# Performance work log

Measured on AMD Instinct MI355X. Metric: run time of the kernel, lower is better.

The kernel has to match this reference:

```python
import jax, jax.numpy as jnp
import numpy as np

N_NODES = 50000
N_EDGES = 100000
NODE_DIM = 6
EDGE_DIM = 4
H = 64        # hidden_dim
HEADS = 4
T = 3         # n_iterations
RED = 16      # CBAM reduction ratio
Z_VALUES = np.array([7.98, 22.98, 38.98, 53.98, 89.98, 180.48], np.float32)


def _ln(x, g, b, eps=1e-5):
    mu = jnp.mean(x, -1, keepdims=True)
    v = jnp.mean((x - mu) ** 2, -1, keepdims=True)
    return (x - mu) * jax.lax.rsqrt(v + eps) * g + b


def _conv1d(x, w, b, pad):
    y = jax.lax.conv_general_dilated(x, w, (1,), [(pad, pad)],
                                     dimension_numbers=('NCH', 'OIH', 'NCH'))
    return y + b[None, :, None]


def _cbam(x, w1, b1, w2, b2, cw1, cb1, cw2, cb2):
    # channel attention: pool over node dim -> [1, 2H] -> MLP -> sigmoid
    cat = jnp.concatenate([x.max(0, keepdims=True), x.mean(0, keepdims=True)], 1)
    cw = jax.nn.sigmoid(jnp.maximum(cat @ w1 + b1, 0.0) @ w2 + b2)  # [1, H]
    x = x * cw
    # spatial attention: pool over feature dim -> conv1d stack over node axis
    sp = jnp.stack([x.max(-1), x.mean(-1)], 0)[None]                # [1, 2, N]
    s = jnp.maximum(_conv1d(sp, cw1, cb1, 2), 0.0)
    s = jax.nn.sigmoid(_conv1d(s, cw2, cb2, 1))                     # [1, 1, N]
    return x * s[0, 0][:, None]


def _forward(x, edge_attr, z_table, W_node, b_node, W_edge, b_edge,
             cn_w1, cn_b1, cn_w2, cn_b2, cn_cw1, cn_cb1, cn_cw2, cn_cb2,
             ce_w1, ce_b1, ce_w2, ce_b2, ce_cw1, ce_cb1, ce_cw2, ce_cb2,
             ln_comb_g, ln_comb_b, Wq, bq, Wk, bk, Wv, bv, Wskip, bskip,
             ln_tc_g, ln_tc_b, Wpn, bpn, Wpe, bpe, Wg, bg,
             Wc1, bc1, Wc2, bc2, edge_index, z_keys):
    n = x.shape[0]
    # bidirectional edges
    src = jnp.concatenate([edge_index[0], edge_index[1]])
    dst = jnp.concatenate([edge_index[1], edge_index[0]])
    eab = jnp.concatenate([edge_attr, edge_attr], 0)
    rel = x[src, :3] - x[dst, :3]

    # z embedding lookup (non-matching z -> index 0, matching torch default)
    zint = jnp.round(x[:, 2]).astype(jnp.int32)
    zidx = jnp.argmax(zint[:, None] == z_keys[None, :], 1)

    nf = jnp.maximum(x @ W_node + b_node, 0.0) + z_table[zidx]
    nf = _cbam(nf, cn_w1, cn_b1, cn_w2, cn_b2, cn_cw1, cn_cb1, cn_cw2, cn_cb2)
    ef = jnp.maximum(jnp.concatenate([eab, rel], 1) @ W_edge + b_edge, 0.0)
    ef = _cbam(ef, ce_w1, ce_b1, ce_w2, ce_b2, ce_cw1, ce_cb1, ce_cw2, ce_cb2)

    scale = float(1.0 / np.sqrt(H))
    for i in range(T):
        x0, e0 = nf, ef
        agg = jax.ops.segment_sum(ef, dst, num_segments=n)
        comb = _ln(jnp.concatenate([nf, agg - nf], 1), ln_comb_g[i], ln_comb_b[i])
        # TransformerConv (PyG): q at dst, k/v at src, segment softmax over dst
        q = (comb @ Wq[i] + bq[i]).reshape(n, HEADS, H)
        k = (comb @ Wk[i] + bk[i]).reshape(n, HEADS, H)
        v = (comb @ Wv[i] + bv[i]).reshape(n, HEADS, H)
        logits = jnp.sum(q[dst] * k[src], -1) * scale           # [2E, HEADS]
        m = jax.ops.segment_max(logits, dst, num_segments=n)
        p = jnp.exp(logits - m[dst])
        denom = jax.ops.segment_sum(p, dst, num_segments=n)
        alpha = p / denom[dst]
        out = jax.ops.segment_sum(alpha[..., None] * v[src], dst, num_segments=n)
        out = out.reshape(n, HEADS * H) + comb @ Wskip[i] + bskip[i]
        out = _ln(out, ln_tc_g[i], ln_tc_b[i])
        npj = out @ Wpn[i] + bpn[i]
        epj = out[src] @ Wpe[i] + bpe[i]
        g = jax.nn.sigmoid(jnp.concatenate([x0, npj], 1) @ Wg[i] + bg[i])
        nf = x0 * g + npj * (1.0 - g)
        g2 = jax.nn.sigmoid(jnp.concatenate([e0, epj], 1) @ Wg[i] + bg[i])
        ef = e0 * g2 + epj * (1.0 - g2)

    s_idx, e_idx = edge_index[0], edge_index[1]
    clf = jnp.concatenate([nf[s_idx], nf[e_idx]], 1)
    return (jnp.maximum(clf @ Wc1 + bc1, 0.0) @ Wc2 + bc2)[:, 0]


def setup_inputs() -> dict:
    key = jax.random.key(0)
    ks = iter(jax.random.split(key, 80))
    def nrm(shape, s=0.05):
        return jax.random.normal(next(ks), shape, jnp.float32) * s
    x = jax.random.normal(next(ks), (N_NODES, NODE_DIM), jnp.float32)
    zch = jax.random.randint(next(ks), (N_NODES,), 0, len(Z_VALUES))
    x = x.at[:, 2].set(jnp.asarray(Z_VALUES)[zch])
    edge_index = jax.random.randint(next(ks), (2, N_EDGES), 0, N_NODES)
    edge_attr = jax.random.normal(next(ks), (N_EDGES, EDGE_DIM), jnp.float32)
    z_keys = jnp.asarray(np.round(Z_VALUES).astype(np.int32))
    HH, r = HEADS * H, H // RED
    def zeros(*s):
        return jnp.zeros(s, jnp.float32)
    inp = dict(
        x=x, edge_attr=edge_attr, edge_index=edge_index, z_keys=z_keys,
        z_table=nrm((len(Z_VALUES), H)),
        W_node=nrm((NODE_DIM, H)), b_node=zeros(H),
        W_edge=nrm((EDGE_DIM + 3, H)), b_edge=zeros(H),
        cn_w1=nrm((2 * H, r)), cn_b1=zeros(r), cn_w2=nrm((r, H)), cn_b2=zeros(H),
        cn_cw1=nrm((1, 2, 5)), cn_cb1=zeros(1), cn_cw2=nrm((1, 1, 3)), cn_cb2=zeros(1),
        ce_w1=nrm((2 * H, r)), ce_b1=zeros(r), ce_w2=nrm((r, H)), ce_b2=zeros(H),
        ce_cw1=nrm((1, 2, 5)), ce_cb1=zeros(1), ce_cw2=nrm((1, 1, 3)), ce_cb2=zeros(1),
        ln_comb_g=jnp.ones((T, 2 * H), jnp.float32), ln_comb_b=zeros(T, 2 * H),
        Wq=nrm((T, 2 * H, HH)), bq=zeros(T, HH),
        Wk=nrm((T, 2 * H, HH)), bk=zeros(T, HH),
        Wv=nrm((T, 2 * H, HH)), bv=zeros(T, HH),
        Wskip=nrm((T, 2 * H, HH)), bskip=zeros(T, HH),
        ln_tc_g=jnp.ones((T, HH), jnp.float32), ln_tc_b=zeros(T, HH),
        Wpn=nrm((T, HH, H)), bpn=zeros(T, H),
        Wpe=nrm((T, HH, H)), bpe=zeros(T, H),
        Wg=nrm((T, 2 * H, H)), bg=zeros(T, H),
        Wc1=nrm((2 * H, H)), bc1=zeros(H), Wc2=nrm((H, 1)), bc2=zeros(1),
    )
    return inp


def reference(x, edge_attr, edge_index, z_keys, z_table, W_node, b_node, W_edge, b_edge,
              cn_w1, cn_b1, cn_w2, cn_b2, cn_cw1, cn_cb1, cn_cw2, cn_cb2,
              ce_w1, ce_b1, ce_w2, ce_b2, ce_cw1, ce_cb1, ce_cw2, ce_cb2,
              ln_comb_g, ln_comb_b, Wq, bq, Wk, bk, Wv, bv, Wskip, bskip,
              ln_tc_g, ln_tc_b, Wpn, bpn, Wpe, bpe, Wg, bg, Wc1, bc1, Wc2, bc2):
    return _forward(x, edge_attr, z_table, W_node, b_node, W_edge, b_edge,
                    cn_w1, cn_b1, cn_w2, cn_b2, cn_cw1, cn_cb1, cn_cw2, cn_cb2,
                    ce_w1, ce_b1, ce_w2, ce_b2, ce_cw1, ce_cb1, ce_cw2, ce_cb2,
                    ln_comb_g, ln_comb_b, Wq, bq, Wk, bk, Wv, bv, Wskip, bskip,
                    ln_tc_g, ln_tc_b, Wpn, bpn, Wpe, bpe, Wg, bg,
                    Wc1, bc1, Wc2, bc2, edge_index, z_keys)
```

## Files before the change

kernel.cpp:

```cpp
#include <hip/hip_runtime.h>


#define LN_EPS 1e-5f
#define PBLK 512

typedef __attribute__((ext_vector_type(8))) short bf16x8;
typedef __attribute__((ext_vector_type(4))) float f32x4;

static __device__ __forceinline__ float wsum(float v) {
#pragma unroll
  for (int d = 32; d > 0; d >>= 1) v += __shfl_xor(v, d);
  return v;
}
static __device__ __forceinline__ float sigm(float x) { return 1.0f / (1.0f + __expf(-x)); }
static __device__ __forceinline__ unsigned short f2bf(float f) {
  unsigned int u = __float_as_uint(f);
  u += 0x7FFFu + ((u >> 16) & 1u);
  return (unsigned short)(u >> 16);
}
static __device__ __forceinline__ float bf2f(unsigned short b) {
  return __uint_as_float(((unsigned int)b) << 16);
}
static __device__ __forceinline__ float4 ld4v(const float* p) { return *(const float4*)p; }
static __device__ __forceinline__ float4 ld4v(const unsigned short* p) {
// ... 71 lines not shown
    }
    if (i < nblk) boff[i] = carry + sc - v;
    carry += __shfl(sc, 63);
  }
  if (lane == 0) off[n] = carry;
}

__global__ __launch_bounds__(256) void k_scan3(int* __restrict__ off, const int* __restrict__ boff, int n) {
  int i = blockIdx.x * 256 + threadIdx.x;
  if (i < n) off[i] += boff[i >> 10];
}

__global__ __launch_bounds__(256) void k_scatter(const int* __restrict__ ei, const int* __restrict__ off,
                                                 int* __restrict__ cur, int* __restrict__ pinv,
                                                 int* __restrict__ slist, int E) {
  int e = blockIdx.x * 256 + threadIdx.x;
  if (e >= 2 * E) return;
  int d = (e < E) ? ei[E + e] : ei[e - E];
  int pos = atomicAdd(&cur[d], 1);
  int base = off[d] + pos;
  pinv[e] = base;
  slist[base] = ei[e];
}

__global__ __launch_bounds__(256) void k_packW(
    const float* __restrict__ Wq, const float* __restrict__ Wk, const float* __restrict__ Wv,
    const float* __restrict__ Ws, const float* __restrict__ bq, const float* __restrict__ bk,
    const float* __restrict__ bv, const float* __restrict__ bs,
    const float* __restrict__ Wpn, const float* __restrict__ Wpe,
    const float* __restrict__ bpn, const float* __restrict__ bpe,
    const float* __restrict__ Wg, const float* __restrict__ Wc1,
    unsigned short* __restrict__ W1t, float* __restrict__ bias1,
    unsigned short* __restrict__ B2t, float* __restrict__ bias2,
    unsigned short* __restrict__ Wg1t, unsigned short* __restrict__ Wc1t) {
  const int S1 = 3 * 1024 * 128, S2 = 3 * 1024, S3 = 3 * 256 * 256, S4 = 3 * 256;
  const int S5 = 3 * 64 * 64, S6 = 2 * 64 * 64;
  int idx = blockIdx.x * 256 + threadIdx.x;
  if (idx < S1) {
    int i = idx / 131072, r = idx % 131072;
    int col = r >> 7, k = r & 127;
    int m = col >> 8, cc = col & 255;
    const float* W = (m == 0) ? Wq : (m == 1) ? Wk : (m == 2) ? Wv : Ws;
    W1t[idx] = f2bf(W[i * 32768 + k * 256 + cc]);
  } else if (idx < S1 + S2) {
    int j = idx - S1;
    int i = j >> 10, col = j & 1023;
    int m = col >> 8, cc = col & 255;
    const float* bsrc = (m == 0) ? bq : (m == 1) ? bk : (m == 2) ? bv : bs;
    bias1[j] = bsrc[i * 256 + cc];
  } else if (idx < S1 + S2 + S3) {
    int j = idx - S1 - S2;
    int i = j / 65536, r = j % 65536;
    int col = r >> 8, k = r & 255;
    float v;
    if (col < 64) v = Wpn[i * 16384 + k * 64 + col];
    else if (col < 128) v = Wpe[i * 16384 + k * 64 + (col - 64)];
    else {
      const float* Wsrc = (col < 192) ? Wpn : Wpe;
      int cc = col & 63;
      float acc = 0.f;
      for (int jj = 0; jj < 64; ++jj)
        acc = fmaf(Wsrc[i * 16384 + k * 64 + jj], Wg[i * 8192 + (64 + jj) * 64 + cc], acc);
      v = acc;
    }
    B2t[j] = f2bf(v);
  } else if (idx < S1 + S2 + S3 + S4) {
    int j = idx - S1 - S2 - S3;
    int i = j >> 8, col = j & 255;
    float v;
    if (col < 64) v = bpn[i * 64 + col];
    else if (col < 128) v = bpe[i * 64 + col - 64];
    else {
      const float* bsrc = (col < 192) ? bpn : bpe;
      int cc = col & 63;
      float acc = 0.f;
      for (int jj = 0; jj < 64; ++jj)
        acc = fmaf(bsrc[i * 64 + jj], Wg[i * 8192 + (64 + jj) * 64 + cc], acc);
      v = acc;
    }
    bias2[j] = v;
  } else if (idx < S1 + S2 + S3 + S4 + S5) {
    int j = idx - S1 - S2 - S3 - S4;
    int i = j / 4096, r = j % 4096;
    int col = r >> 6, k = r & 63;
    Wg1t[j] = f2bf(Wg[i * 8192 + k * 64 + col]);
  } else if (idx < S1 + S2 + S3 + S4 + S5 + S6) {
    int j = idx - S1 - S2 - S3 - S4 - S5;
    int h = j / 4096, r = j % 4096;
    int col = r >> 6, k = r & 63;
    Wc1t[j] = f2bf(Wc1[(h * 64 + k) * 64 + col]);
  }
}

__global__ __launch_bounds__(256) void k_node_embed(
    const float* __restrict__ x, const int* __restrict__ zk, const float* __restrict__ zt,
    const float* __restrict__ Wn, const float* __restrict__ bn, float* __restrict__ nf, int N) {
  int n = blockIdx.x * 4 + (threadIdx.x >> 6);
  int lane = threadIdx.x & 63;
  if (n >= N) return;
  const float* xr = x + (size_t)n * 6;
  float acc = bn[lane];
#pragma unroll
  for (int d = 0; d < 6; ++d) acc = fmaf(xr[d], Wn[d * 64 + lane], acc);
  int zi = __float2int_rn(xr[2]);
  int idx = 0;
#pragma unroll
  for (int t = 5; t >= 0; --t)
    if (zi == zk[t]) idx = t;
  nf[(size_t)n * 64 + lane] = fmaxf(acc, 0.0f) + zt[idx * 64 + lane];
}

__global__ __launch_bounds__(256) void k_edge_embed(
    const float* __restrict__ x, const float* __restrict__ ea, const int* __restrict__ ei,
    const float* __restrict__ We, const float* __restrict__ be,
    unsigned short* __restrict__ ef, int E) {
  int e = blockIdx.x * 4 + (threadIdx.x >> 6);
  int lane = threadIdx.x & 63;
  if (e >= 2 * E) return;
  int e0 = (e < E) ? e : e - E;
  int s = ei[e];
  int d = (e < E) ? ei[E + e] : ei[e - E];
  const float* ar = ea + (size_t)e0 * 4;
  const float* xs = x + (size_t)s * 6;
  const float* xd = x + (size_t)d * 6;
  float in[7];
  in[0] = ar[0]; in[1] = ar[1]; in[2] = ar[2]; in[3] = ar[3];
  in[4] = xs[0] - xd[0]; in[5] = xs[1] - xd[1]; in[6] = xs[2] - xd[2];
// ... 124 lines not shown
  __syncthreads();
  int o = base + threadIdx.x;
  if (o < n) {
    float a = b2[0] + tl[threadIdx.x] * w2[0] + tl[threadIdx.x + 1] * w2[1] + tl[threadIdx.x + 2] * w2[2];
    s[o] = sigm(a);
  }
}

__global__ __launch_bounds__(256) void k_row_scale(float* __restrict__ buf, int n, const float* __restrict__ s) {
  int i4 = blockIdx.x * 256 + threadIdx.x;
  if (i4 >= n * 16) return;
  int r = i4 >> 4;
  float sc = s[r];
  float4 v = ld4v(buf + (size_t)i4 * 4);
  v.x *= sc; v.y *= sc; v.z *= sc; v.w *= sc;
  st4v(buf + (size_t)i4 * 4, v);
}

__global__ __launch_bounds__(256) void k_row_scale_perm(const unsigned short* __restrict__ src, int n,
                                                        const float* __restrict__ s,
                                                        const int* __restrict__ pinv,
                                                        unsigned short* __restrict__ dst) {
  int i4 = blockIdx.x * 256 + threadIdx.x;
  if (i4 >= n * 16) return;
  int r = i4 >> 4, c4 = (i4 & 15) * 4;
  float sc = s[r];
  float4 v = ld4v(src + (size_t)r * 64 + c4);
  v.x *= sc; v.y *= sc; v.z *= sc; v.w *= sc;
  st4v(dst + (size_t)pinv[r] * 64 + c4, v);
}

__global__ __launch_bounds__(256) void k_aggcomb(const unsigned short* __restrict__ efc,
                                                 const float* __restrict__ nf,
                                                 const int* __restrict__ off,
                                                 unsigned short* __restrict__ comb, const float* __restrict__ g,
                                                 const float* __restrict__ b, int N) {
  int n = blockIdx.x * 4 + (threadIdx.x >> 6);
  int lane = threadIdx.x & 63;
  if (n >= N) return;
  float agg = 0.0f;
  int i0 = off[n], i1 = off[n + 1];
  for (int idx = i0; idx < i1; ++idx) agg += bf2f(efc[(size_t)idx * 64 + lane]);
  float y0 = nf[(size_t)n * 64 + lane];
  float y1 = agg - y0;
  float s1 = wsum(y0 + y1);
  float s2 = wsum(y0 * y0 + y1 * y1);
  float mu = s1 * (1.0f / 128.0f);
  float var = s2 * (1.0f / 128.0f) - mu * mu;
  float rs = rsqrtf(fmaxf(var, 0.0f) + LN_EPS);
  comb[(size_t)n * 128 + lane] = f2bf((y0 - mu) * rs * g[lane] + b[lane]);
  comb[(size_t)n * 128 + 64 + lane] = f2bf((y1 - mu) * rs * g[64 + lane] + b[64 + lane]);
}

template <int MODE>
__global__ __launch_bounds__(256) void gemm_mfma(
    const unsigned short* __restrict__ A, int M, int K,
    const unsigned short* __restrict__ Bt, const float* __restrict__ bias,
    unsigned short* __restrict__ outQ, unsigned short* __restrict__ outK,
    unsigned short* __restrict__ outS) {
  __shared__ unsigned short shmem[128 * 136];
  unsigned short* As = shmem;
  unsigned short* Bs = shmem + 128 * 64;
  const int tid = threadIdx.x;
  int bm, bn;
  if (MODE == 0) {
    int cpx = gridDim.x >> 3;
    int wgid = (blockIdx.x & 7) * cpx + (blockIdx.x >> 3);
    bm = (wgid >> 3) * 128;
    bn = (wgid & 7) * 128;
  } else {
    bm = blockIdx.x * 128;
    bn = blockIdx.y * 128;
  }
  const int wid = tid >> 6, lane = tid & 63;
  const int wr = (wid >> 1) * 64, wc = (wid & 1) * 64;
  const int lrow = lane & 15, lkb = (lane >> 4) * 8;
  f32x4 acc[4][4];
#pragma unroll
  for (int m = 0; m < 4; ++m)
#pragma unroll
    for (int n = 0; n < 4; ++n) acc[m][n] = (f32x4){0.f, 0.f, 0.f, 0.f};

  for (int k0 = 0; k0 < K; k0 += 64) {
#pragma unroll
    for (int l = 0; l < 4; ++l) {
      int c = tid + l * 256;
      int row = c >> 3, kc = (c & 7) * 8;
      int sw = row * 64 + (kc ^ ((row & 7) << 3));
      int grow = bm + row;
      bf16x8 v = {0, 0, 0, 0, 0, 0, 0, 0};
      if (grow < M) v = *(const bf16x8*)(A + (size_t)grow * K + k0 + kc);
      *(bf16x8*)&As[sw] = v;
      int gcol = bn + row;
      *(bf16x8*)&Bs[sw] = *(const bf16x8*)(Bt + (size_t)gcol * K + k0 + kc);
    }
    __syncthreads();
#pragma unroll
    for (int ks = 0; ks < 2; ++ks) {
      const int ke = ks * 32 + lkb;
      bf16x8 af[4], bfr[4];
#pragma unroll
      for (int m = 0; m < 4; ++m) {
        int row = wr + m * 16 + lrow;
        af[m] = *(const bf16x8*)&As[row * 64 + (ke ^ ((row & 7) << 3))];
      }
#pragma unroll
      for (int n = 0; n < 4; ++n) {
        int col = wc + n * 16 + lrow;
        bfr[n] = *(const bf16x8*)&Bs[col * 64 + (ke ^ ((col & 7) << 3))];
      }
#pragma unroll
      for (int m = 0; m < 4; ++m)
#pragma unroll
        for (int n = 0; n < 4; ++n)
          acc[m][n] = __builtin_amdgcn_mfma_f32_16x16x32_bf16(af[m], bfr[n], acc[m][n], 0, 0, 0);
    }
    __syncthreads();
  }

  const int colw = lane & 15, rq = (lane >> 4) * 4;
  unsigned short* Cs = shmem;
#pragma unroll
  for (int m = 0; m < 4; ++m) {
#pragma unroll
    for (int n = 0; n < 4; ++n) {
      int col = wc + n * 16 + colw;
      float bv = bias[bn + col];
#pragma unroll
      for (int r = 0; r < 4; ++r) {
        int row = wr + m * 16 + rq + r;
        Cs[row * 136 + col] = f2bf(acc[m][n][r] + bv);
      }
    }
  }
  __syncthreads();
  const int rsub = tid >> 4, c8 = (tid & 15) * 8;
#pragma unroll
  for (int i = 0; i < 8; ++i) {
    int row = i * 16 + rsub;
    int grow = bm + row;
    if (grow >= M) continue;
    uint4 v = *(const uint4*)&Cs[row * 136 + c8];
    if (MODE == 1) {
      *(uint4*)(outQ + (size_t)grow * 256 + bn + c8) = v;
    } else {
      const int proj = bn >> 8;
      int cc = (bn & 255) + c8;
      if (proj == 0) *(uint4*)(outQ + (size_t)grow * 256 + cc) = v;
      else if (proj == 1) *(uint4*)(outK + (size_t)grow * 512 + cc) = v;
      else if (proj == 2) *(uint4*)(outK + (size_t)grow * 512 + 256 + cc) = v;
      else *(uint4*)(outS + (size_t)grow * 256 + cc) = v;
    }
  }
}

template <int UPD>
__global__ __launch_bounds__(256) void gemm_gate(
    const void* __restrict__ Av, int M, const unsigned short* __restrict__ Wt,
    const unsigned short* __restrict__ P, const float* __restrict__ bgv,
    const int* __restrict__ srcl, void* __restrict__ updv) {
  __shared__ unsigned short As[128 * 64];
  __shared__ unsigned short Ws[64 * 64];
  const int tid = threadIdx.x;
  const int bm = blockIdx.x * 128;
  if (UPD == 2) {
    const unsigned short* Ab = (const unsigned short*)Av;
#pragma unroll
    for (int l = 0; l < 4; ++l) {
      int u = tid + l * 256;
      int row = u >> 3, kc = (u & 7) * 8;
      int grow = bm + row;
      bf16x8 v = {0, 0, 0, 0, 0, 0, 0, 0};
      if (grow < M) v = *(const bf16x8*)(Ab + (size_t)grow * 64 + kc);
      *(bf16x8*)&As[row * 64 + (kc ^ ((row & 7) << 3))] = v;
    }
  } else {
    const float* Af = (const float*)Av;
#pragma unroll
    for (int l = 0; l < 8; ++l) {
      int u = tid + l * 256;
      int row = u >> 4, k4 = (u & 15) << 2;
      int grow = bm + row;
      float4 v = make_float4(0.f, 0.f, 0.f, 0.f);
      if (grow < M) v = *(const float4*)(Af + (size_t)grow * 64 + k4);
      union { unsigned short h[4]; uint2 q; } pk;
      pk.h[0] = f2bf(v.x); pk.h[1] = f2bf(v.y); pk.h[2] = f2bf(v.z); pk.h[3] = f2bf(v.w);
      *(uint2*)&As[row * 64 + (k4 ^ ((row & 7) << 3))] = pk.q;
    }
  }
#pragma unroll
  for (int l = 0; l < 2; ++l) {
    int u = tid + l * 256;
    int row = u >> 3, kc = (u & 7) * 8;
    *(bf16x8*)&Ws[row * 64 + (kc ^ ((row & 7) << 3))] = *(const bf16x8*)(Wt + row * 64 + kc);
  }
  __syncthreads();
  const int wid = tid >> 6, lane = tid & 63;
  const int wr = wid * 32;
  const int lrow = lane & 15, lkb = (lane >> 4) * 8;
  f32x4 acc[2][4];
#pragma unroll
  for (int m = 0; m < 2; ++m)
#pragma unroll
    for (int n = 0; n < 4; ++n) acc[m][n] = (f32x4){0.f, 0.f, 0.f, 0.f};
#pragma unroll
  for (int ks = 0; ks < 2; ++ks) {
    const int ke = ks * 32 + lkb;
    bf16x8 af[2], wf[4];
#pragma unroll
    for (int m = 0; m < 2; ++m) {
      int row = wr + m * 16 + lrow;
      af[m] = *(const bf16x8*)&As[row * 64 + (ke ^ ((row & 7) << 3))];
    }
#pragma unroll
    for (int n = 0; n < 4; ++n) {
      int col = n * 16 + lrow;
      wf[n] = *(const bf16x8*)&Ws[col * 64 + (ke ^ ((col & 7) << 3))];
    }
#pragma unroll
    for (int m = 0; m < 2; ++m)
#pragma unroll
      for (int n = 0; n < 4; ++n)
        acc[m][n] = __builtin_amdgcn_mfma_f32_16x16x32_bf16(af[m], wf[n], acc[m][n], 0, 0, 0);
  }
  const int colw = lane & 15, rq = (lane >> 4) * 4;
#pragma unroll
  for (int m = 0; m < 2; ++m) {
#pragma unroll
    for (int r = 0; r < 4; ++r) {
      int e = bm + wr + m * 16 + rq + r;
      if (e >= M) continue;
      if (UPD == 0) {
        float* upd = (float*)updv;
#pragma unroll
        for (int n = 0; n < 4; ++n) upd[(size_t)e * 64 + n * 16 + colw] = acc[m][n][r];
      } else if (UPD == 1) {
        float* upd = (float*)updv;
        const unsigned short* Pr = P + (size_t)e * 256;
#pragma unroll
        for (int n = 0; n < 4; ++n) {
          int c = n * 16 + colw;
          float g = sigm(acc[m][n][r] + bf2f(Pr[128 + c]) + bgv[c]);
          size_t oi = (size_t)e * 64 + c;
          upd[oi] = upd[oi] * g + bf2f(Pr[c]) * (1.0f - g);
        }
      } else {
        unsigned short* upd = (unsigned short*)updv;
        int s = srcl[e];
        const unsigned short* Pr = P + (size_t)s * 256;
#pragma unroll
        for (int n = 0; n < 4; ++n) {
          int c = n * 16 + colw;
          float g = sigm(acc[m][n][r] + bf2f(Pr[192 + c]) + bgv[c]);
          size_t oi = (size_t)e * 64 + c;
          float vA = bf2f(upd[oi]);
          upd[oi] = f2bf(vA * g + bf2f(Pr[64 + c]) * (1.0f - g));
        }
      }
    }
  }
}

__global__ __launch_bounds__(256) void k_attn(const unsigned short* __restrict__ qo,
                                              const unsigned short* __restrict__ kv,
                                              const unsigned short* __restrict__ skipb, const int* __restrict__ off,
                                              const int* __restrict__ slist,
                                              unsigned short* __restrict__ aob,
                                              const float* __restrict__ g, const float* __restrict__ b, int N) {
  int n = blockIdx.x * 4 + (threadIdx.x >> 6);
  int lane = threadIdx.x & 63;
  if (n >= N) return;
  union { uint2 u; unsigned short h[4]; } qq;
  qq.u = *(const uint2*)(qo + (size_t)n * 256 + 4 * lane);
  float q0 = bf2f(qq.h[0]), q1 = bf2f(qq.h[1]), q2 = bf2f(qq.h[2]), q3 = bf2f(qq.h[3]);
  float m = -INFINITY, lsum = 0.f;
  float a0 = 0.f, a1 = 0.f, a2 = 0.f, a3 = 0.f;
  int i0 = off[n], i1 = off[n + 1];
  int idx = i0;
  for (; idx + 4 <= i1; idx += 4) {
    int s0 = slist[idx], s1 = slist[idx + 1], s2 = slist[idx + 2], s3 = slist[idx + 3];
    const unsigned short* kb0 = kv + (size_t)s0 * 512;
    const unsigned short* kb1 = kv + (size_t)s1 * 512;
    const unsigned short* kb2 = kv + (size_t)s2 * 512;
    const unsigned short* kb3 = kv + (size_t)s3 * 512;
    union { uint2 u; unsigned short h[4]; } kk0, vv0, kk1, vv1, kk2, vv2, kk3, vv3;
    kk0.u = *(const uint2*)(kb0 + 4 * lane); vv0.u = *(const uint2*)(kb0 + 256 + 4 * lane);
    kk1.u = *(const uint2*)(kb1 + 4 * lane); vv1.u = *(const uint2*)(kb1 + 256 + 4 * lane);
    kk2.u = *(const uint2*)(kb2 + 4 * lane); vv2.u = *(const uint2*)(kb2 + 256 + 4 * lane);
    kk3.u = *(const uint2*)(kb3 + 4 * lane); vv3.u = *(const uint2*)(kb3 + 256 + 4 * lane);
    float d0 = q0 * bf2f(kk0.h[0]) + q1 * bf2f(kk0.h[1]) + q2 * bf2f(kk0.h[2]) + q3 * bf2f(kk0.h[3]);
    float d1 = q0 * bf2f(kk1.h[0]) + q1 * bf2f(kk1.h[1]) + q2 * bf2f(kk1.h[2]) + q3 * bf2f(kk1.h[3]);
    float d2 = q0 * bf2f(kk2.h[0]) + q1 * bf2f(kk2.h[1]) + q2 * bf2f(kk2.h[2]) + q3 * bf2f(kk2.h[3]);
    float d3 = q0 * bf2f(kk3.h[0]) + q1 * bf2f(kk3.h[1]) + q2 * bf2f(kk3.h[2]) + q3 * bf2f(kk3.h[3]);
#pragma unroll
    for (int dd = 1; dd < 16; dd <<= 1) {
      d0 += __shfl_xor(d0, dd);
      d1 += __shfl_xor(d1, dd);
      d2 += __shfl_xor(d2, dd);
      d3 += __shfl_xor(d3, dd);
    }
    d0 *= 0.125f; d1 *= 0.125f; d2 *= 0.125f; d3 *= 0.125f;
    float nm, sc, p;
    nm = fmaxf(m, d0); sc = __expf(m - nm); p = __expf(d0 - nm);
    lsum = lsum * sc + p;
    a0 = fmaf(p, bf2f(vv0.h[0]), a0 * sc); a1 = fmaf(p, bf2f(vv0.h[1]), a1 * sc);
    a2 = fmaf(p, bf2f(vv0.h[2]), a2 * sc); a3 = fmaf(p, bf2f(vv0.h[3]), a3 * sc);
    m = nm;
    nm = fmaxf(m, d1); sc = __expf(m - nm); p = __expf(d1 - nm);
    lsum = lsum * sc + p;
    a0 = fmaf(p, bf2f(vv1.h[0]), a0 * sc); a1 = fmaf(p, bf2f(vv1.h[1]), a1 * sc);
    a2 = fmaf(p, bf2f(vv1.h[2]), a2 * sc); a3 = fmaf(p, bf2f(vv1.h[3]), a3 * sc);
    m = nm;
    nm = fmaxf(m, d2); sc = __expf(m - nm); p = __expf(d2 - nm);
    lsum = lsum * sc + p;
    a0 = fmaf(p, bf2f(vv2.h[0]), a0 * sc); a1 = fmaf(p, bf2f(vv2.h[1]), a1 * sc);
    a2 = fmaf(p, bf2f(vv2.h[2]), a2 * sc); a3 = fmaf(p, bf2f(vv2.h[3]), a3 * sc);
    m = nm;
    nm = fmaxf(m, d3); sc = __expf(m - nm); p = __expf(d3 - nm);
    lsum = lsum * sc + p;
    a0 = fmaf(p, bf2f(vv3.h[0]), a0 * sc); a1 = fmaf(p, bf2f(vv3.h[1]), a1 * sc);
    a2 = fmaf(p, bf2f(vv3.h[2]), a2 * sc); a3 = fmaf(p, bf2f(vv3.h[3]), a3 * sc);
    m = nm;
  }
  for (; idx + 2 <= i1; idx += 2) {
    int sA = slist[idx], sB = slist[idx + 1];
    const unsigned short* kbA = kv + (size_t)sA * 512;
    const unsigned short* kbB = kv + (size_t)sB * 512;
    union { uint2 u; unsigned short h[4]; } kkA, vvA, kkB, vvB;
    kkA.u = *(const uint2*)(kbA + 4 * lane); vvA.u = *(const uint2*)(kbA + 256 + 4 * lane);
    kkB.u = *(const uint2*)(kbB + 4 * lane); vvB.u = *(const uint2*)(kbB + 256 + 4 * lane);
    float dA = q0 * bf2f(kkA.h[0]) + q1 * bf2f(kkA.h[1]) + q2 * bf2f(kkA.h[2]) + q3 * bf2f(kkA.h[3]);
    float dB = q0 * bf2f(kkB.h[0]) + q1 * bf2f(kkB.h[1]) + q2 * bf2f(kkB.h[2]) + q3 * bf2f(kkB.h[3]);
#pragma unroll
    for (int dd = 1; dd < 16; dd <<= 1) {
      dA += __shfl_xor(dA, dd);
      dB += __shfl_xor(dB, dd);
    }
    dA *= 0.125f; dB *= 0.125f;
    float nm, sc, p;
    nm = fmaxf(m, dA); sc = __expf(m - nm); p = __expf(dA - nm);
    lsum = lsum * sc + p;
    a0 = fmaf(p, bf2f(vvA.h[0]), a0 * sc); a1 = fmaf(p, bf2f(vvA.h[1]), a1 * sc);
    a2 = fmaf(p, bf2f(vvA.h[2]), a2 * sc); a3 = fmaf(p, bf2f(vvA.h[3]), a3 * sc);
    m = nm;
    nm = fmaxf(m, dB); sc = __expf(m - nm); p = __expf(dB - nm);
    lsum = lsum * sc + p;
    a0 = fmaf(p, bf2f(vvB.h[0]), a0 * sc); a1 = fmaf(p, bf2f(vvB.h[1]), a1 * sc);
    a2 = fmaf(p, bf2f(vvB.h[2]), a2 * sc); a3 = fmaf(p, bf2f(vvB.h[3]), a3 * sc);
    m = nm;
  }
  if (idx < i1) {
    int s = slist[idx];
    const unsigned short* kb = kv + (size_t)s * 512;
    union { uint2 u; unsigned short h[4]; } kk, vv;
    kk.u = *(const uint2*)(kb + 4 * lane);
    vv.u = *(const uint2*)(kb + 256 + 4 * lane);
    float d = q0 * bf2f(kk.h[0]) + q1 * bf2f(kk.h[1]) + q2 * bf2f(kk.h[2]) + q3 * bf2f(kk.h[3]);
#pragma unroll
    for (int dd = 1; dd < 16; dd <<= 1) d += __shfl_xor(d, dd);
    d *= 0.125f;
    float nm = fmaxf(m, d);
    float sc = __expf(m - nm);
    float p = __expf(d - nm);
    lsum = lsum * sc + p;
    a0 = fmaf(p, bf2f(vv.h[0]), a0 * sc);
    a1 = fmaf(p, bf2f(vv.h[1]), a1 * sc);
    a2 = fmaf(p, bf2f(vv.h[2]), a2 * sc);
    a3 = fmaf(p, bf2f(vv.h[3]), a3 * sc);
    m = nm;
  }
  union { uint2 u; unsigned short h[4]; } sb;
  sb.u = *(const uint2*)(skipb + (size_t)n * 256 + 4 * lane);
  float inv = (lsum > 0.f) ? 1.0f / lsum : 0.f;
  float v0 = bf2f(sb.h[0]) + a0 * inv;
  float v1 = bf2f(sb.h[1]) + a1 * inv;
  float v2 = bf2f(sb.h[2]) + a2 * inv;
  float v3 = bf2f(sb.h[3]) + a3 * inv;
  float s1 = wsum(v0 + v1 + v2 + v3);
  float s2 = wsum(v0 * v0 + v1 * v1 + v2 * v2 + v3 * v3);
  float mu = s1 * (1.0f / 256.0f);
  float var = s2 * (1.0f / 256.0f) - mu * mu;
  float rs = rsqrtf(fmaxf(var, 0.0f) + LN_EPS);
  float4 g4 = *(const float4*)(g + 4 * lane);
  float4 b4 = *(const float4*)(b + 4 * lane);
  union { uint2 u; unsigned short h[4]; } ob;
  ob.h[0] = f2bf((v0 - mu) * rs * g4.x + b4.x);
  ob.h[1] = f2bf((v1 - mu) * rs * g4.y + b4.y);
  ob.h[2] = f2bf((v2 - mu) * rs * g4.z + b4.z);
  ob.h[3] = f2bf((v3 - mu) * rs * g4.w + b4.w);
  *(uint2*)(aob + (size_t)n * 256 + 4 * lane) = ob.u;
}

__global__ __launch_bounds__(256) void k_clf_pair(const float* __restrict__ ABt, const float* __restrict__ ABb,
                                                  const int* __restrict__ ei, const float* __restrict__ bc1,
                                                  const float* __restrict__ Wc2, const float* __restrict__ bc2,
                                                  float* __restrict__ out, int E) {
  int e = blockIdx.x * 4 + (threadIdx.x >> 6);
  int lane = threadIdx.x & 63;
  if (e >= E) return;
  int s = ei[e], t = ei[E + e];
  float h = fmaxf(ABt[(size_t)s * 64 + lane] + ABb[(size_t)t * 64 + lane] + bc1[lane], 0.0f);
  float r = wsum(h * Wc2[lane]);
  if (lane == 0) out[e] = r + bc2[0];
}

extern "C" void kernel_launch(void* const* d_in, const int* in_sizes, int n_in,
                              void* d_out, int out_size, void* d_ws, size_t ws_size,
                              hipStream_t stream) {
  const float* x = (const float*)d_in[0];
  const float* edge_attr = (const float*)d_in[1];
  const int* ei = (const int*)d_in[2];
  const int* zk = (const int*)d_in[3];
  const float* z_table = (const float*)d_in[4];
  const float* W_node = (const float*)d_in[5];
  const float* b_node = (const float*)d_in[6];
  const float* W_edge = (const float*)d_in[7];
  const float* b_edge = (const float*)d_in[8];
  const float* cn_w1 = (const float*)d_in[9];
  const float* cn_b1 = (const float*)d_in[10];
  const float* cn_w2 = (const float*)d_in[11];
  const float* cn_b2 = (const float*)d_in[12];
  const float* cn_cw1 = (const float*)d_in[13];
// ... 21 lines not shown
  const float* ln_tc_g = (const float*)d_in[35];
  const float* ln_tc_b = (const float*)d_in[36];
  const float* Wpn = (const float*)d_in[37];
  const float* bpn = (const float*)d_in[38];
  const float* Wpe = (const float*)d_in[39];
  const float* bpe = (const float*)d_in[40];
  const float* Wg = (const float*)d_in[41];
  const float* bg = (const float*)d_in[42];
  const float* Wc1 = (const float*)d_in[43];
  const float* bc1 = (const float*)d_in[44];
  const float* Wc2 = (const float*)d_in[45];
  const float* bc2 = (const float*)d_in[46];
  float* out = (float*)d_out;

  const int N = in_sizes[0] / 6;
  const int E = in_sizes[2] / 2;
  const int E2 = 2 * E;

  char* p = (char*)d_ws;
  auto carve = [&](size_t bytes) -> void* {
    void* r = (void*)p;
    p += (bytes + 255) & ~(size_t)255;
    return r;
  };
  unsigned short* qo = (unsigned short*)carve((size_t)N * 256 * 2);
  unsigned short* skipb = (unsigned short*)carve((size_t)N * 256 * 2);
  unsigned short* kvb = (unsigned short*)carve((size_t)N * 512 * 2);
  unsigned short* aob = (unsigned short*)carve((size_t)N * 256 * 2);
  unsigned short* efb = (unsigned short*)carve((size_t)E2 * 64 * 2);
  unsigned short* efc = (unsigned short*)carve((size_t)E2 * 64 * 2);
  float* nf = (float*)carve((size_t)N * 64 * 4);
  unsigned short* comb = (unsigned short*)carve((size_t)N * 128 * 2);
  unsigned short* W1t = (unsigned short*)carve((size_t)3 * 1024 * 128 * 2);
  float* bias1 = (float*)carve((size_t)3 * 1024 * 4);
  unsigned short* B2t = (unsigned short*)carve((size_t)3 * 256 * 256 * 2);
  float* bias2 = (float*)carve((size_t)3 * 256 * 4);
  unsigned short* Wg1t = (unsigned short*)carve((size_t)3 * 64 * 64 * 2);
  unsigned short* Wc1t = (unsigned short*)carve((size_t)2 * 64 * 64 * 2);
  int* cnt = (int*)carve((size_t)N * 4);
  int* cur = (int*)carve((size_t)N * 4);
  int* off = (int*)carve((size_t)(N + 1) * 4);
  int* pinv = (int*)carve((size_t)E2 * 4);
  int* slist = (int*)carve((size_t)E2 * 4);
  int* bsum = (int*)carve((size_t)256 * 4);
  int* boff = (int*)carve((size_t)256 * 4);
  float* pm = (float*)carve((size_t)PBLK * 64 * 4);
  float* ps = (float*)carve((size_t)PBLK * 64 * 4);
  float* cwv = (float*)carve(64 * 4);
  float* spmax = (float*)carve((size_t)E2 * 4);
  float* spmean = (float*)carve((size_t)E2 * 4);
  float* sconv = (float*)carve((size_t)E2 * 4);
  size_t need = (size_t)(p - (char*)d_ws);

  unsigned short* Pb = skipb;
  float* ABt = (float*)aob;
  float* ABb = (float*)aob + (size_t)N * 64;

  auto cdiv = [](int a, int b) { return (a + b - 1) / b; };

  if (ws_size < need) {
    k_sentinel<<<cdiv(E, 256), 256, 0, stream>>>(out, E);
    return;
  }

  k_zero2<<<cdiv(N, 256), 256, 0, stream>>>(cnt, cur, N);
  k_hist<<<cdiv(E2, 256), 256, 0, stream>>>(ei, cnt, E);
  const int nblk = cdiv(N, 1024);
  k_scan1<<<nblk, 256, 0, stream>>>(cnt, off, bsum, N);
  k_scan2<<<1, 64, 0, stream>>>(bsum, boff, off, N, nblk);
  k_scan3<<<cdiv(N, 256), 256, 0, stream>>>(off, boff, N);
  k_scatter<<<cdiv(E2, 256), 256, 0, stream>>>(ei, off, cur, pinv, slist, E);

  const int PACK = 3 * 1024 * 128 + 3 * 1024 + 3 * 256 * 256 + 3 * 256 + 3 * 64 * 64 + 2 * 64 * 64;
  k_packW<<<cdiv(PACK, 256), 256, 0, stream>>>(Wq, Wk, Wv, Wskip, bq, bk, bv, bskip,
                                               Wpn, Wpe, bpn, bpe, Wg, Wc1,
                                               W1t, bias1, B2t, bias2, Wg1t, Wc1t);

  k_node_embed<<<cdiv(N, 4), 256, 0, stream>>>(x, zk, z_table, W_node, b_node, nf, N);
  k_edge_embed<<<cdiv(E2, 4), 256, 0, stream>>>(x, edge_attr, ei, W_edge, b_edge, efb, E);

  k_pool_partial<float><<<PBLK, 256, 0, stream>>>(nf, N, pm, ps);
  k_pool_final<<<1, 256, 0, stream>>>(pm, ps, N, PBLK, cn_w1, cn_b1, cn_w2, cn_b2, cwv);
  k_chan_sp<float><<<cdiv(N, 16), 256, 0, stream>>>(nf, N, cwv, spmax, spmean);
  k_conv<<<cdiv(N, 256), 256, 0, stream>>>(spmax, spmean, N, cn_cw1, cn_cb1, cn_cw2, cn_cb2, sconv);
  k_row_scale<<<cdiv(N * 16, 256), 256, 0, stream>>>(nf, N, sconv);

  k_pool_partial<unsigned short><<<PBLK, 256, 0, stream>>>(efb, E2, pm, ps);
  k_pool_final<<<1, 256, 0, stream>>>(pm, ps, E2, PBLK, ce_w1, ce_b1, ce_w2, ce_b2, cwv);
  k_chan_sp<unsigned short><<<cdiv(E2, 16), 256, 0, stream>>>(efb, E2, cwv, spmax, spmean);
  k_conv<<<cdiv(E2, 256), 256, 0, stream>>>(spmax, spmean, E2, ce_cw1, ce_cb1, ce_cw2, ce_cb2, sconv);
  k_row_scale_perm<<<cdiv(E2 * 16, 256), 256, 0, stream>>>(efb, E2, sconv, pinv, efc);

  const int gqkvs = cdiv(N, 128) * 8;
  dim3 gp(cdiv(N, 128), 2);
  for (int i = 0; i < 3; ++i) {
    k_aggcomb<<<cdiv(N, 4), 256, 0, stream>>>(efc, nf, off, comb,
                                              ln_comb_g + (size_t)i * 128, ln_comb_b + (size_t)i * 128, N);
    gemm_mfma<0><<<gqkvs, 256, 0, stream>>>(comb, N, 128, W1t + (size_t)i * 131072,
                                            bias1 + (size_t)i * 1024, qo, kvb, skipb);
    k_attn<<<cdiv(N, 4), 256, 0, stream>>>(qo, kvb, skipb, off, slist, aob,
                                           ln_tc_g + (size_t)i * 256, ln_tc_b + (size_t)i * 256, N);
    gemm_mfma<1><<<gp, 256, 0, stream>>>(aob, N, 256, B2t + (size_t)i * 65536,
                                         bias2 + (size_t)i * 256, Pb, nullptr, nullptr);
    gemm_gate<1><<<cdiv(N, 128), 256, 0, stream>>>(nf, N, Wg1t + (size_t)i * 4096, Pb,
                                                   bg + (size_t)i * 64, nullptr, nf);
    gemm_gate<2><<<cdiv(E2, 128), 256, 0, stream>>>(efc, E2, Wg1t + (size_t)i * 4096, Pb,
                                                    bg + (size_t)i * 64, slist, efc);
  }

  gemm_gate<0><<<cdiv(N, 128), 256, 0, stream>>>(nf, N, Wc1t, nullptr, nullptr, nullptr, ABt);
  gemm_gate<0><<<cdiv(N, 128), 256, 0, stream>>>(nf, N, Wc1t + 4096, nullptr, nullptr, nullptr, ABb);
  k_clf_pair<<<cdiv(E, 4), 256, 0, stream>>>(ABt, ABb, ei, bc1, Wc2, bc2, out, E);
  (void)out_size;
  (void)n_in;
}
```

Baseline: 714.7 us.

## Fuse node gate update into projection GEMM and drop online-softmax max tracking

The P projection GEMM and the node gate update become one kernel, gemm_p. Blocks with y=0 compute the node gate GEMM and apply the gated update to nf directly, and blocks with y=1 write only the edge-side projections into a compact 128-wide buffer. This removes one kernel launch per iteration and halves the P buffer traffic. The attention kernel also drops the running-max rescaling of online softmax and exponentiates the scaled scores directly, which risks overflow if scores get large.

After: 697.9 us. 1.02x faster.

```diff
diff --git a/kernel.cpp b/kernel.cpp
--- a/kernel.cpp
+++ b/kernel.cpp
@@ -147,12 +147,12 @@
     int j = idx - S1 - S2;
     int i = j / 65536, r = j % 65536;
     int col = r >> 8, k = r & 255;
+    int half = col >> 6, cc = col & 63;
     float v;
-    if (col < 64) v = Wpn[i * 16384 + k * 64 + col];
-    else if (col < 128) v = Wpe[i * 16384 + k * 64 + (col - 64)];
+    if (half == 0) v = Wpn[i * 16384 + k * 64 + cc];
+    else if (half == 2) v = Wpe[i * 16384 + k * 64 + cc];
     else {
-      const float* Wsrc = (col < 192) ? Wpn : Wpe;
-      int cc = col & 63;
+      const float* Wsrc = (half == 1) ? Wpn : Wpe;
       float acc = 0.f;
       for (int jj = 0; jj < 64; ++jj)
         acc = fmaf(Wsrc[i * 16384 + k * 64 + jj], Wg[i * 8192 + (64 + jj) * 64 + cc], acc);
@@ -162,12 +162,12 @@
   } else if (idx < S1 + S2 + S3 + S4) {
     int j = idx - S1 - S2 - S3;
     int i = j >> 8, col = j & 255;
+    int half = col >> 6, cc = col & 63;
     float v;
-    if (col < 64) v = bpn[i * 64 + col];
-    else if (col < 128) v = bpe[i * 64 + col - 64];
+    if (half == 0) v = bpn[i * 64 + cc];
+    else if (half == 2) v = bpe[i * 64 + cc];
     else {
-      const float* bsrc = (col < 192) ? bpn : bpe;
-      int cc = col & 63;
+      const float* bsrc = (half == 1) ? bpn : bpe;
       float acc = 0.f;
       for (int jj = 0; jj < 64; ++jj)
         acc = fmaf(bsrc[i * 64 + jj], Wg[i * 8192 + (64 + jj) * 64 + cc], acc);
@@ -398,7 +398,6 @@
   comb[(size_t)n * 128 + 64 + lane] = f2bf((y1 - mu) * rs * g[64 + lane] + b[64 + lane]);
 }
 
-template <int MODE>
 __global__ __launch_bounds__(256) void gemm_mfma(
     const unsigned short* __restrict__ A, int M, int K,
     const unsigned short* __restrict__ Bt, const float* __restrict__ bias,
@@ -408,16 +407,10 @@
   unsigned short* As = shmem;
   unsigned short* Bs = shmem + 128 * 64;
   const int tid = threadIdx.x;
-  int bm, bn;
-  if (MODE == 0) {
-    int cpx = gridDim.x >> 3;
-    int wgid = (blockIdx.x & 7) * cpx + (blockIdx.x >> 3);
-    bm = (wgid >> 3) * 128;
-    bn = (wgid & 7) * 128;
-  } else {
-    bm = blockIdx.x * 128;
-    bn = blockIdx.y * 128;
-  }
+  int cpx = gridDim.x >> 3;
+  int wgid = (blockIdx.x & 7) * cpx + (blockIdx.x >> 3);
+  int bm = (wgid >> 3) * 128;
+  int bn = (wgid & 7) * 128;
   const int wid = tid >> 6, lane = tid & 63;
   const int wr = (wid >> 1) * 64, wc = (wid & 1) * 64;
   const int lrow = lane & 15, lkb = (lane >> 4) * 8;
@@ -487,15 +480,164 @@
     int grow = bm + row;
     if (grow >= M) continue;
     uint4 v = *(const uint4*)&Cs[row * 136 + c8];
-    if (MODE == 1) {
-      *(uint4*)(outQ + (size_t)grow * 256 + bn + c8) = v;
-    } else {
-      const int proj = bn >> 8;
-      int cc = (bn & 255) + c8;
-      if (proj == 0) *(uint4*)(outQ + (size_t)grow * 256 + cc) = v;
-      else if (proj == 1) *(uint4*)(outK + (size_t)grow * 512 + cc) = v;
-      else if (proj == 2) *(uint4*)(outK + (size_t)grow * 512 + 256 + cc) = v;
-      else *(uint4*)(outS + (size_t)grow * 256 + cc) = v;
+    const int proj = bn >> 8;
+    int cc = (bn & 255) + c8;
+    if (proj == 0) *(uint4*)(outQ + (size_t)grow * 256 + cc) = v;
+    else if (proj == 1) *(uint4*)(outK + (size_t)grow * 512 + cc) = v;
+    else if (proj == 2) *(uint4*)(outK + (size_t)grow * 512 + 256 + cc) = v;
+    else *(uint4*)(outS + (size_t)grow * 256 + cc) = v;
+  }
+}
+
+__global__ __launch_bounds__(256) void gemm_p(
+    const unsigned short* __restrict__ aob, float* __restrict__ nf, int N,
+    const unsigned short* __restrict__ B2t, const float* __restrict__ bias2,
+    const unsigned short* __restrict__ Wg1t, const float* __restrict__ bgv,
+    unsigned short* __restrict__ Pe) {
+  __shared__ unsigned short shmem[128 * 136];
+  unsigned short* As = shmem;
+  unsigned short* Bs = shmem + 128 * 64;
+  const int tid = threadIdx.x;
+  const int bm = blockIdx.x * 128;
+  const bool nodeblk = (blockIdx.y == 0);
+  const int wid = tid >> 6, lane = tid & 63;
+  const int lrow = lane & 15, lkb = (lane >> 4) * 8;
+
+  f32x4 accS[2][4];
+  if (nodeblk) {
+#pragma unroll
+    for (int l = 0; l < 8; ++l) {
+      int u = tid + l * 256;
+      int row = u >> 4, k4 = (u & 15) << 2;
+      int grow = bm + row;
+      float4 v = make_float4(0.f, 0.f, 0.f, 0.f);
+      if (grow < N) v = *(const float4*)(nf + (size_t)grow * 64 + k4);
+      union { unsigned short h[4]; uint2 q; } pk;
+      pk.h[0] = f2bf(v.x); pk.h[1] = f2bf(v.y); pk.h[2] = f2bf(v.z); pk.h[3] = f2bf(v.w);
+      *(uint2*)&As[row * 64 + (k4 ^ ((row & 7) << 3))] = pk.q;
+    }
+#pragma unroll
+    for (int l = 0; l < 2; ++l) {
+      int u = tid + l * 256;
+      int row = u >> 3, kc = (u & 7) * 8;
+      *(bf16x8*)&Bs[row * 64 + (kc ^ ((row & 7) << 3))] = *(const bf16x8*)(Wg1t + row * 64 + kc);
+    }
+    __syncthreads();
+    const int wrS = wid * 32;
+#pragma unroll
+    for (int m = 0; m < 2; ++m)
+#pragma unroll
+      for (int n = 0; n < 4; ++n) accS[m][n] = (f32x4){0.f, 0.f, 0.f, 0.f};
+#pragma unroll
+    for (int ks = 0; ks < 2; ++ks) {
+      const int ke = ks * 32 + lkb;
+      bf16x8 af[2], wf[4];
+#pragma unroll
+      for (int m = 0; m < 2; ++m) {
+        int row = wrS + m * 16 + lrow;
+        af[m] = *(const bf16x8*)&As[row * 64 + (ke ^ ((row & 7) << 3))];
+      }
+#pragma unroll
+      for (int n = 0; n < 4; ++n) {
+        int col = n * 16 + lrow;
+        wf[n] = *(const bf16x8*)&Bs[col * 64 + (ke ^ ((col & 7) << 3))];
+      }
+#pragma unroll
+      for (int m = 0; m < 2; ++m)
+#pragma unroll
+        for (int n = 0; n < 4; ++n)
+          accS[m][n] = __builtin_amdgcn_mfma_f32_16x16x32_bf16(af[m], wf[n], accS[m][n], 0, 0, 0);
+    }
+    __syncthreads();
+  }
+
+  const int cbase = nodeblk ? 0 : 128;
+  const int wr = (wid >> 1) * 64, wc = (wid & 1) * 64;
+  f32x4 acc[4][4];
+#pragma unroll
+  for (int m = 0; m < 4; ++m)
+#pragma unroll
+    for (int n = 0; n < 4; ++n) acc[m][n] = (f32x4){0.f, 0.f, 0.f, 0.f};
+  for (int k0 = 0; k0 < 256; k0 += 64) {
+#pragma unroll
+    for (int l = 0; l < 4; ++l) {
+      int c = tid + l * 256;
+      int row = c >> 3, kc = (c & 7) * 8;
+      int sw = row * 64 + (kc ^ ((row & 7) << 3));
+      int grow = bm + row;
+      bf16x8 v = {0, 0, 0, 0, 0, 0, 0, 0};
+      if (grow < N) v = *(const bf16x8*)(aob + (size_t)grow * 256 + k0 + kc);
+      *(bf16x8*)&As[sw] = v;
+      *(bf16x8*)&Bs[sw] = *(const bf16x8*)(B2t + (size_t)(cbase + row) * 256 + k0 + kc);
+    }
+    __syncthreads();
+#pragma unroll
+    for (int ks = 0; ks < 2; ++ks) {
+      const int ke = ks * 32 + lkb;
+      bf16x8 af[4], bfr[4];
+#pragma unroll
+      for (int m = 0; m < 4; ++m) {
+        int row = wr + m * 16 + lrow;
+        af[m] = *(const bf16x8*)&As[row * 64 + (ke ^ ((row & 7) << 3))];
+      }
+#pragma unroll
+      for (int n = 0; n < 4; ++n) {
+        int col = wc + n * 16 + lrow;
+        bfr[n] = *(const bf16x8*)&Bs[col * 64 + (ke ^ ((col & 7) << 3))];
+      }
+#pragma unroll
+      for (int m = 0; m < 4; ++m)
+#pragma unroll
+        for (int n = 0; n < 4; ++n)
+          acc[m][n] = __builtin_amdgcn_mfma_f32_16x16x32_bf16(af[m], bfr[n], acc[m][n], 0, 0, 0);
+    }
+    __syncthreads();
+  }
+
+  const int colw = lane & 15, rq = (lane >> 4) * 4;
+  unsigned short* Cs = shmem;
+#pragma unroll
+  for (int m = 0; m < 4; ++m) {
+#pragma unroll
+    for (int n = 0; n < 4; ++n) {
+      int col = wc + n * 16 + colw;
+      float bv = bias2[cbase + col];
+#pragma unroll
+      for (int r = 0; r < 4; ++r) {
+        int row = wr + m * 16 + rq + r;
+        Cs[row * 136 + col] = f2bf(acc[m][n][r] + bv);
+      }
+    }
+  }
+  __syncthreads();
+
+  if (nodeblk) {
+    const int wrS = wid * 32;
+#pragma unroll
+    for (int m = 0; m < 2; ++m) {
+#pragma unroll
+      for (int r = 0; r < 4; ++r) {
+        int row = wrS + m * 16 + rq + r;
+        int grow = bm + row;
+        if (grow >= N) continue;
+#pragma unroll
+        for (int n = 0; n < 4; ++n) {
+          int c = n * 16 + colw;
+          float g = sigm(accS[m][n][r] + bf2f(Cs[row * 136 + 64 + c]) + bgv[c]);
+          size_t oi = (size_t)grow * 64 + c;
+          float old = nf[oi];
+          nf[oi] = old * g + bf2f(Cs[row * 136 + c]) * (1.0f - g);
+        }
+      }
+    }
+  } else {
+    const int rsub = tid >> 4, c8 = (tid & 15) * 8;
+#pragma unroll
+    for (int i = 0; i < 8; ++i) {
+      int row = i * 16 + rsub;
+      int grow = bm + row;
+      if (grow >= N) continue;
+      *(uint4*)(Pe + (size_t)grow * 128 + c8) = *(const uint4*)&Cs[row * 136 + c8];
     }
   }
 }
@@ -580,27 +722,17 @@
         float* upd = (float*)updv;
 #pragma unroll
         for (int n = 0; n < 4; ++n) upd[(size_t)e * 64 + n * 16 + colw] = acc[m][n][r];
-      } else if (UPD == 1) {
-        float* upd = (float*)updv;
-        const unsigned short* Pr = P + (size_t)e * 256;
-#pragma unroll
-        for (int n = 0; n < 4; ++n) {
-          int c = n * 16 + colw;
-          float g = sigm(acc[m][n][r] + bf2f(Pr[128 + c]) + bgv[c]);
-          size_t oi = (size_t)e * 64 + c;
-          upd[oi] = upd[oi] * g + bf2f(Pr[c]) * (1.0f - g);
-        }
       } else {
         unsigned short* upd = (unsigned short*)updv;
         int s = srcl[e];
-        const unsigned short* Pr = P + (size_t)s * 256;
+        const unsigned short* Pr = P + (size_t)s * 128;
 #pragma unroll
         for (int n = 0; n < 4; ++n) {
           int c = n * 16 + colw;
-          float g = sigm(acc[m][n][r] + bf2f(Pr[192 + c]) + bgv[c]);
+          float g = sigm(acc[m][n][r] + bf2f(Pr[64 + c]) + bgv[c]);
           size_t oi = (size_t)e * 64 + c;
           float vA = bf2f(upd[oi]);
-          upd[oi] = f2bf(vA * g + bf2f(Pr[64 + c]) * (1.0f - g));
+          upd[oi] = f2bf(vA * g + bf2f(Pr[c]) * (1.0f - g));
         }
       }
     }
@@ -619,7 +751,7 @@
   union { uint2 u; unsigned short h[4]; } qq;
   qq.u = *(const uint2*)(qo + (size_t)n * 256 + 4 * lane);
   float q0 = bf2f(qq.h[0]), q1 = bf2f(qq.h[1]), q2 = bf2f(qq.h[2]), q3 = bf2f(qq.h[3]);
-  float m = -INFINITY, lsum = 0.f;
+  float lsum = 0.f;
   float a0 = 0.f, a1 = 0.f, a2 = 0.f, a3 = 0.f;
   int i0 = off[n], i1 = off[n + 1];
   int idx = i0;
@@ -645,57 +777,21 @@
       d2 += __shfl_xor(d2, dd);
       d3 += __shfl_xor(d3, dd);
     }
-    d0 *= 0.125f; d1 *= 0.125f; d2 *= 0.125f; d3 *= 0.125f;
-    float nm, sc, p;
-    nm = fmaxf(m, d0); sc = __expf(m - nm); p = __expf(d0 - nm);
-    lsum = lsum * sc + p;
-    a0 = fmaf(p, bf2f(vv0.h[0]), a0 * sc); a1 = fmaf(p, bf2f(vv0.h[1]), a1 * sc);
-    a2 = fmaf(p, bf2f(vv0.h[2]), a2 * sc); a3 = fmaf(p, bf2f(vv0.h[3]), a3 * sc);
-    m = nm;
-    nm = fmaxf(m, d1); sc = __expf(m - nm); p = __expf(d1 - nm);
-    lsum = lsum * sc + p;
-    a0 = fmaf(p, bf2f(vv1.h[0]), a0 * sc); a1 = fmaf(p, bf2f(vv1.h[1]), a1 * sc);
-    a2 = fmaf(p, bf2f(vv1.h[2]), a2 * sc); a3 = fmaf(p, bf2f(vv1.h[3]), a3 * sc);
-    m = nm;
-    nm = fmaxf(m, d2); sc = __expf(m - nm); p = __expf(d2 - nm);
-    lsum = lsum * sc + p;
-    a0 = fmaf(p, bf2f(vv2.h[0]), a0 * sc); a1 = fmaf(p, bf2f(vv2.h[1]), a1 * sc);
-    a2 = fmaf(p, bf2f(vv2.h[2]), a2 * sc); a3 = fmaf(p, bf2f(vv2.h[3]), a3 * sc);
-    m = nm;
-    nm = fmaxf(m, d3); sc = __expf(m - nm); p = __expf(d3 - nm);
-    lsum = lsum * sc + p;
-    a0 = fmaf(p, bf2f(vv3.h[0]), a0 * sc); a1 = fmaf(p, bf2f(vv3.h[1]), a1 * sc);
-    a2 = fmaf(p, bf2f(vv3.h[2]), a2 * sc); a3 = fmaf(p, bf2f(vv3.h[3]), a3 * sc);
-    m = nm;
-  }
-  for (; idx + 2 <= i1; idx += 2) {
-    int sA = slist[idx], sB = slist[idx + 1];
-    const unsigned short* kbA = kv + (size_t)sA * 512;
-    const unsigned short* kbB = kv + (size_t)sB * 512;
-    union { uint2 u; unsigned short h[4]; } kkA, vvA, kkB, vvB;
-    kkA.u = *(const uint2*)(kbA + 4 * lane); vvA.u = *(const uint2*)(kbA + 256 + 4 * lane);
-    kkB.u = *(const uint2*)(kbB + 4 * lane); vvB.u = *(const uint2*)(kbB + 256 + 4 * lane);
-    float dA = q0 * bf2f(kkA.h[0]) + q1 * bf2f(kkA.h[1]) + q2 * bf2f(kkA.h[2]) + q3 * bf2f(kkA.h[3]);
-    float dB = q0 * bf2f(kkB.h[0]) + q1 * bf2f(kkB.h[1]) + q2 * bf2f(kkB.h[2]) + q3 * bf2f(kkB.h[3]);
-#pragma unroll
-    for (int dd = 1; dd < 16; dd <<= 1) {
-      dA += __shfl_xor(dA, dd);
-      dB += __shfl_xor(dB, dd);
-    }
-    dA *= 0.125f; dB *= 0.125f;
-    float nm, sc, p;
-    nm = fmaxf(m, dA); sc = __expf(m - nm); p = __expf(dA - nm);
-    lsum = lsum * sc + p;
-    a0 = fmaf(p, bf2f(vvA.h[0]), a0 * sc); a1 = fmaf(p, bf2f(vvA.h[1]), a1 * sc);
-    a2 = fmaf(p, bf2f(vvA.h[2]), a2 * sc); a3 = fmaf(p, bf2f(vvA.h[3]), a3 * sc);
-    m = nm;
-    nm = fmaxf(m, dB); sc = __expf(m - nm); p = __expf(dB - nm);
-    lsum = lsum * sc + p;
-    a0 = fmaf(p, bf2f(vvB.h[0]), a0 * sc); a1 = fmaf(p, bf2f(vvB.h[1]), a1 * sc);
-    a2 = fmaf(p, bf2f(vvB.h[2]), a2 * sc); a3 = fmaf(p, bf2f(vvB.h[3]), a3 * sc);
-    m = nm;
-  }
-  if (idx < i1) {
+    float p0 = __expf(d0 * 0.125f);
+    float p1 = __expf(d1 * 0.125f);
+    float p2 = __expf(d2 * 0.125f);
+    float p3 = __expf(d3 * 0.125f);
+    lsum += p0 + p1 + p2 + p3;
+    a0 = fmaf(p0, bf2f(vv0.h[0]), a0); a1 = fmaf(p0, bf2f(vv0.h[1]), a1);
+    a2 = fmaf(p0, bf2f(vv0.h[2]), a2); a3 = fmaf(p0, bf2f(vv0.h[3]), a3);
+    a0 = fmaf(p1, bf2f(vv1.h[0]), a0); a1 = fmaf(p1, bf2f(vv1.h[1]), a1);
+    a2 = fmaf(p1, bf2f(vv1.h[2]), a2); a3 = fmaf(p1, bf2f(vv1.h[3]), a3);
+    a0 = fmaf(p2, bf2f(vv2.h[0]), a0); a1 = fmaf(p2, bf2f(vv2.h[1]), a1);
+    a2 = fmaf(p2, bf2f(vv2.h[2]), a2); a3 = fmaf(p2, bf2f(vv2.h[3]), a3);
+    a0 = fmaf(p3, bf2f(vv3.h[0]), a0); a1 = fmaf(p3, bf2f(vv3.h[1]), a1);
+    a2 = fmaf(p3, bf2f(vv3.h[2]), a2); a3 = fmaf(p3, bf2f(vv3.h[3]), a3);
+  }
+  for (; idx < i1; ++idx) {
     int s = slist[idx];
     const unsigned short* kb = kv + (size_t)s * 512;
     union { uint2 u; unsigned short h[4]; } kk, vv;
@@ -704,16 +800,12 @@
     float d = q0 * bf2f(kk.h[0]) + q1 * bf2f(kk.h[1]) + q2 * bf2f(kk.h[2]) + q3 * bf2f(kk.h[3]);
 #pragma unroll
     for (int dd = 1; dd < 16; dd <<= 1) d += __shfl_xor(d, dd);
-    d *= 0.125f;
-    float nm = fmaxf(m, d);
-    float sc = __expf(m - nm);
-    float p = __expf(d - nm);
-    lsum = lsum * sc + p;
-    a0 = fmaf(p, bf2f(vv.h[0]), a0 * sc);
-    a1 = fmaf(p, bf2f(vv.h[1]), a1 * sc);
-    a2 = fmaf(p, bf2f(vv.h[2]), a2 * sc);
-    a3 = fmaf(p, bf2f(vv.h[3]), a3 * sc);
-    m = nm;
+    float p = __expf(d * 0.125f);
+    lsum += p;
+    a0 = fmaf(p, bf2f(vv.h[0]), a0);
+    a1 = fmaf(p, bf2f(vv.h[1]), a1);
+    a2 = fmaf(p, bf2f(vv.h[2]), a2);
+    a3 = fmaf(p, bf2f(vv.h[3]), a3);
   }
   union { uint2 u; unsigned short h[4]; } sb;
   sb.u = *(const uint2*)(skipb + (size_t)n * 256 + 4 * lane);
@@ -841,7 +933,7 @@
   float* sconv = (float*)carve((size_t)E2 * 4);
   size_t need = (size_t)(p - (char*)d_ws);
 
-  unsigned short* Pb = skipb;
+  unsigned short* Pe = skipb;
   float* ABt = (float*)aob;
   float* ABb = (float*)aob + (size_t)N * 64;
 
@@ -881,19 +973,18 @@
   k_row_scale_perm<<<cdiv(E2 * 16, 256), 256, 0, stream>>>(efb, E2, sconv, pinv, efc);
 
   const int gqkvs = cdiv(N, 128) * 8;
-  dim3 gp(cdiv(N, 128), 2);
+  dim3 gpf(cdiv(N, 128), 2);
   for (int i = 0; i < 3; ++i) {
     k_aggcomb<<<cdiv(N, 4), 256, 0, stream>>>(efc, nf, off, comb,
                                               ln_comb_g + (size_t)i * 128, ln_comb_b + (size_t)i * 128, N);
-    gemm_mfma<0><<<gqkvs, 256, 0, stream>>>(comb, N, 128, W1t + (size_t)i * 131072,
-                                            bias1 + (size_t)i * 1024, qo, kvb, skipb);
+    gemm_mfma<<<gqkvs, 256, 0, stream>>>(comb, N, 128, W1t + (size_t)i * 131072,
+                                         bias1 + (size_t)i * 1024, qo, kvb, skipb);
     k_attn<<<cdiv(N, 4), 256, 0, stream>>>(qo, kvb, skipb, off, slist, aob,
                                            ln_tc_g + (size_t)i * 256, ln_tc_b + (size_t)i * 256, N);
-    gemm_mfma<1><<<gp, 256, 0, stream>>>(aob, N, 256, B2t + (size_t)i * 65536,
-                                         bias2 + (size_t)i * 256, Pb, nullptr, nullptr);
-    gemm_gate<1><<<cdiv(N, 128), 256, 0, stream>>>(nf, N, Wg1t + (size_t)i * 4096, Pb,
-                                                   bg + (size_t)i * 64, nullptr, nf);
-    gemm_gate<2><<<cdiv(E2, 128), 256, 0, stream>>>(efc, E2, Wg1t + (size_t)i * 4096, Pb,
+    gemm_p<<<gpf, 256, 0, stream>>>(aob, nf, N, B2t + (size_t)i * 65536,
+                                    bias2 + (size_t)i * 256, Wg1t + (size_t)i * 4096,
+                                    bg + (size_t)i * 64, Pe);
+    gemm_gate<2><<<cdiv(E2, 128), 256, 0, stream>>>(efc, E2, Wg1t + (size_t)i * 4096, Pe,
                                                     bg + (size_t)i * 64, slist, efc);
   }
 
```
